# Optimization experiments

Hardware: AMD Instinct MI355X
Metric: run time of the kernel (lower is better)

Reference implementation:

```python
import jax, jax.numpy as jnp
import numpy as np

L, H, D, DH, DFF, V, P, T, R = 12, 12, 768, 64, 3072, 30522, 512, 2, 50
RAT_LAYER = 6  # original condition: 5 < idx < 7


def layer_norm(x, g, b, eps=1e-12):
    m = x.mean(-1, keepdims=True)
    v = ((x - m) ** 2).mean(-1, keepdims=True)
    return (x - m) / jnp.sqrt(v + eps) * g + b


def setup_inputs() -> dict:
    key = jax.random.key(0)
    ks = iter(jax.random.split(key, 20))
    def n(shape, s=0.02):
        return jax.random.normal(next(ks), shape, dtype=jnp.float32) * s
    inp = dict(
        input_ids=jax.random.randint(next(ks), (4, 512), 0, V, dtype=jnp.int32),
        relations=jax.random.randint(next(ks), (4, 512, 512), 0, R, dtype=jnp.int32),
        attention_mask=jnp.ones((4, 512), dtype=jnp.int32),
        word_emb=n((V, D)), pos_emb=n((P, D)), type_emb=n((T, D)),
        emb_ln_g=jnp.ones((D,)), emb_ln_b=jnp.zeros((D,)),
        Wq=n((L, D, D)), bq=jnp.zeros((L, D)), Wk=n((L, D, D)), bk=jnp.zeros((L, D)),
        Wv=n((L, D, D)), bv=jnp.zeros((L, D)), Wo=n((L, D, D)), bo=jnp.zeros((L, D)),
        ln1_g=jnp.ones((L, D)), ln1_b=jnp.zeros((L, D)),
        Wi=n((L, D, DFF)), bi=jnp.zeros((L, DFF)),
        Wf=n((L, DFF, D)), bf=jnp.zeros((L, D)),
        ln2_g=jnp.ones((L, D)), ln2_b=jnp.zeros((L, D)),
        key_rel=n((L, R, DH)), val_rel=n((L, R, DH)),
        pool_w=n((D, D)), pool_b=jnp.zeros((D,)),
    )
    return inp


def reference(input_ids, relations, attention_mask, word_emb, pos_emb, type_emb,
              emb_ln_g, emb_ln_b, Wq, bq, Wk, bk, Wv, bv, Wo, bo, ln1_g, ln1_b,
              Wi, bi, Wf, bf, ln2_g, ln2_b, key_rel, val_rel, pool_w, pool_b):
    B, S = input_ids.shape
    # BERT embeddings (token_type_ids = zeros as in module default)
    h = word_emb[input_ids] + pos_emb[jnp.arange(S)][None] + type_emb[0][None, None]
    h = layer_norm(h, emb_ln_g, emb_ln_b)
    ext_mask = (1.0 - attention_mask.astype(jnp.float32))[:, None, None, :] * -10000.0
    inv_sqrt_dh = np.float32(1.0 / np.sqrt(DH))
    for i in range(L):
        q = (h @ Wq[i] + bq[i]).reshape(B, S, H, DH).transpose(0, 2, 1, 3)
        k = (h @ Wk[i] + bk[i]).reshape(B, S, H, DH).transpose(0, 2, 1, 3)
        v = (h @ Wv[i] + bv[i]).reshape(B, S, H, DH).transpose(0, 2, 1, 3)
        scores = jnp.einsum('bhsd,bhtd->bhst', q, k)
        if i == RAT_LAYER:
            kr = key_rel[i][relations]            # [B,S,S,DH] gathered relation keys
            scores = scores + jnp.einsum('bhsd,bstd->bhst', q, kr)
        scores = scores * inv_sqrt_dh + ext_mask
        probs = jax.nn.softmax(scores, axis=-1)   # dropout = identity (eval)
        ctx = jnp.einsum('bhst,bhtd->bhsd', probs, v)
        if i == RAT_LAYER:
            vr = val_rel[i][relations]            # [B,S,S,DH] gathered relation values
            ctx = ctx + jnp.einsum('bhst,bstd->bhsd', probs, vr)
        ctx = ctx.transpose(0, 2, 1, 3).reshape(B, S, D)
        attn_out = layer_norm(ctx @ Wo[i] + bo[i] + h, ln1_g[i], ln1_b[i])
        ff = jax.nn.gelu(attn_out @ Wi[i] + bi[i], approximate=False)
        h = layer_norm(ff @ Wf[i] + bf[i] + attn_out, ln2_g[i], ln2_b[i])
    pooled = jnp.tanh(h[:, 0] @ pool_w + pool_b)
    return h, pooled
```

## Files before the change

kernel.cpp:

```cpp
#include <hip/hip_runtime.h>
#include <math.h>

typedef unsigned short u16;
typedef unsigned int   u32;
typedef __bf16  bf16x8 __attribute__((ext_vector_type(8)));
typedef float   f32x4  __attribute__((ext_vector_type(4)));
typedef u16     u16x8  __attribute__((ext_vector_type(8)));
typedef u16     u16x4  __attribute__((ext_vector_type(4)));

__device__ __forceinline__ u16 f2bf(float f) {
  u32 u = __builtin_bit_cast(u32, f);
  u32 r = (u + 0x7fffu + ((u >> 16) & 1u)) >> 16;
  return (u16)r;
}
__device__ __forceinline__ float bf2f(u16 h) {
  u32 u = ((u32)h) << 16;
  return __builtin_bit_cast(float, u);
}
__device__ __forceinline__ void gload16(const void* g, void* l) {
  __builtin_amdgcn_global_load_lds((const __attribute__((address_space(1))) void*)g,
                                   (__attribute__((address_space(3))) void*)l, 16, 0, 0);
}
__device__ __forceinline__ bf16x8 ld_bf8(const u16* p) {
  u16x8 v = *(const u16x8*)p;
  return __builtin_bit_cast(bf16x8, v);
}
__device__ __forceinline__ f32x4 mfma16(bf16x8 a, bf16x8 b, f32x4 c) {
  return __builtin_amdgcn_mfma_f32_16x16x32_bf16(a, b, c, 0, 0, 0);
}

struct ConvP {
  const float *wq, *wk, *wv, *wo, *wi, *wf;
  u16 *oqkv, *oo, *oi, *of;
  long doqkv, doo, doi, dof;
};
__global__ __launch_bounds__(256) void conv_weights(ConvP p, int l0) {
  int l = l0 + blockIdx.x / 6912;
  int t = blockIdx.x % 6912;
  const float* in; u16* out; int K, N, tn, tk;
  if (t < 1728) { int wh = t / 576, tt = t % 576;
    in = (wh==0 ? p.wq : (wh==1 ? p.wk : p.wv)) + (size_t)l*768*768;
    out = p.oqkv + (size_t)l*p.doqkv + (size_t)wh * 768 * 768;
    K = 768; N = 768; tn = tt % 24; tk = tt / 24;
  } else if (t < 2304) { int tt = t - 1728;
    in = p.wo + (size_t)l*768*768; out = p.oo + (size_t)l*p.doo;
    K=768;  N=768;  tn=tt%24; tk=tt/24;
  } else if (t < 4608) { int tt = t - 2304;
    in = p.wi + (size_t)l*768*3072; out = p.oi + (size_t)l*p.doi;
    K=768;  N=3072; tn=tt%96; tk=tt/96;
  } else { int tt = t - 4608;
    in = p.wf + (size_t)l*768*3072; out = p.of + (size_t)l*p.dof;
    K=3072; N=768;  tn=tt%24; tk=tt/24;
  }
  int n0 = tn*32, k0 = tk*32;
  __shared__ float tile[32][33];
  int tx = threadIdx.x, ty = threadIdx.y;
  float4 rv = *(const float4*)(in + (size_t)(k0 + ty) * N + n0 + tx*4);
  tile[ty][tx*4+0] = rv.x; tile[ty][tx*4+1] = rv.y;
  tile[ty][tx*4+2] = rv.z; tile[ty][tx*4+3] = rv.w;
  __syncthreads();
  u16x4 ov;
  ov[0] = f2bf(tile[tx*4+0][ty]); ov[1] = f2bf(tile[tx*4+1][ty]);
  ov[2] = f2bf(tile[tx*4+2][ty]); ov[3] = f2bf(tile[tx*4+3][ty]);
  *(u16x4*)(out + (size_t)(n0 + ty) * K + k0 + tx*4) = ov;
}

struct GP {
  const u16* A; const u16* B;
  int K, N;
  long sA, sB, sOut;
  const float* bias; const float* res;
  float* outF; u16* outB;
  const float* bq; const float* bk; const float* bv;
  u16* qO; u16* kO; u16* vO;
};

template<int BM, int BN, int WAVES, int EPI, int KS>
__global__ __launch_bounds__(WAVES*64) void gemm_bt(GP p) {
  constexpr int THREADS = WAVES * 64;
  constexpr int WC = WAVES / 2;
  constexpr int WM = BM / 2, WN = BN / WC, MR = WM / 16, NR = WN / 16;
  constexpr int AIT = BM * 64 / (THREADS * 8);
  constexpr int BIT = BN * 64 / (THREADS * 8);
  const int tid = threadIdx.x;
  const int wave = tid >> 6, lane = tid & 63;
  const int wr = wave / WC, wc = wave % WC;
  const int wm0 = wr * WM, wn0 = wc * WN;
  const int bn = blockIdx.x, bm = blockIdx.y, bz = blockIdx.z;
  const int K = p.K;
  const int kLen = K / KS;
  const int kBeg = (KS > 1) ? bz * kLen : 0;
  const u16* A  = p.A + ((KS > 1) ? 0 : (size_t)bz * p.sA);
  const u16* Bp = p.B + ((KS > 1) ? 0 : (size_t)bz * p.sB);
  const int rowA0 = bm * BM, colB0 = bn * BN;

  __shared__ __align__(16) u16 lds[(BM + BN) * 64];
  u16* Al = lds; u16* Bl = lds + BM * 64;

  f32x4 acc[MR][NR];
  #pragma unroll
  for (int i = 0; i < MR; ++i)
    #pragma unroll
    for (int j = 0; j < NR; ++j) acc[i][j] = f32x4{0.f,0.f,0.f,0.f};

  for (int kt = kBeg; kt < kBeg + kLen; kt += 64) {
    #pragma unroll
    for (int it = 0; it < AIT; ++it) {
      int e = tid * 8 + it * THREADS * 8;
      gload16(A + (size_t)(rowA0 + (e >> 6)) * K + kt + (e & 63), Al + e);
    }
    #pragma unroll
    for (int it = 0; it < BIT; ++it) {
      int e = tid * 8 + it * THREADS * 8;
      gload16(Bp + (size_t)(colB0 + (e >> 6)) * K + kt + (e & 63), Bl + e);
    }
    __syncthreads();
    #pragma unroll
    for (int ks = 0; ks < 2; ++ks) {
      bf16x8 av[MR]; bf16x8 bw[NR];
      #pragma unroll
      for (int mf = 0; mf < MR; ++mf)
        av[mf] = ld_bf8(Al + (wm0 + mf*16 + (lane&15))*64 + ks*32 + (lane>>4)*8);
      #pragma unroll
      for (int nf = 0; nf < NR; ++nf)
        bw[nf] = ld_bf8(Bl + (wn0 + nf*16 + (lane&15))*64 + ks*32 + (lane>>4)*8);
      #pragma unroll
      for (int mf = 0; mf < MR; ++mf)
        #pragma unroll
        for (int nf = 0; nf < NR; ++nf)
          acc[mf][nf] = mfma16(av[mf], bw[nf], acc[mf][nf]);
    }
    __syncthreads();
  }

  #pragma unroll
  for (int mf = 0; mf < MR; ++mf) {
    #pragma unroll
    for (int nf = 0; nf < NR; ++nf) {
      int col = colB0 + wn0 + nf*16 + (lane & 15);
      #pragma unroll
      for (int reg = 0; reg < 4; ++reg) {
        int row = rowA0 + wm0 + mf*16 + (lane >> 4)*4 + reg;
        float v = acc[mf][nf][reg];
        if constexpr (EPI == 0) {
          int wh = col / 768, cc = col % 768;
          int hh = cc >> 6, d = col & 63;
          int b = row >> 9, s = row & 511;
          const float* bias = wh==0 ? p.bq : (wh==1 ? p.bk : p.bv);
          u16 o = f2bf(v + bias[cc]);
          if (wh == 0)      p.qO[((((size_t)b*12 + hh)*512 + s) << 6) + d] = o;
          else if (wh == 1) p.kO[((((size_t)b*12 + hh)*512 + s) << 6) + d] = o;
          else              p.vO[((((size_t)b*12 + hh)*64  + d) << 9) + s] = o;
        } else if constexpr (EPI == 2) {
          p.outF[(size_t)bz * p.sOut + (size_t)row * p.N + col] = v;
        } else {
          float xg = v + p.bias[col];
          float gg = 0.5f * xg * (1.f + erff(xg * 0.70710678118f));
          p.outB[(size_t)row * p.N + col] = f2bf(gg);
        }
      }
    }
  }
}

template<int RAT>
__global__ __launch_bounds__(256) void flash_attn(
    const u16* __restrict__ q, const u16* __restrict__ k, const u16* __restrict__ v,
    const int* __restrict__ mask, u16* __restrict__ ctx,
    const float* __restrict__ qr, const int* __restrict__ rel,
    float* __restrict__ wbins) {
  const int head = blockIdx.x;
  const int bm = blockIdx.y;
  const int b = head / 12, hh = head % 12;
  const int tid = threadIdx.x, wave = tid >> 6, lane = tid & 63;
  const int wr = wave >> 1, wc = wave & 1;
  const int row0 = bm * 32;
  const u16* qb = q + (size_t)head * 512 * 64;
  const u16* kb = k + (size_t)head * 512 * 64;
  const u16* vb = v + (size_t)head * 64 * 512;

  __shared__ __align__(16) u16 Kl[2][64*64];
  __shared__ __align__(16) u16 Vl[2][64*64];
  __shared__ __align__(16) u16 pw[4][16*72];
  __shared__ float em_lds[512];
  __shared__ float mlb[2][16][2];
  __shared__ float qlds[RAT ? 32 : 1][RAT ? 52 : 1];
  __shared__ float wlds[RAT ? 2 : 1][RAT ? 32 : 1][RAT ? 50 : 1];
  __shared__ float scl[RAT ? 2 : 1][RAT ? 32 : 1];
  __shared__ float aex[RAT ? 32 : 1][RAT ? 3 : 1];

  for (int i = tid; i < 512; i += 256)
    em_lds[i] = -10000.f * (1.f - (float)mask[b*512 + i]);
  if constexpr (RAT) {
    for (int i = tid; i < 2*32*50; i += 256) ((float*)wlds)[i] = 0.f;
    for (int i = tid; i < 32*50; i += 256) {
      int rr = i % 50, sr = i / 50;
      qlds[sr][rr] = qr[((size_t)head*512 + row0 + sr)*50 + rr];
    }
  }

  const int qrow = row0 + wr*16 + (lane & 15);
  bf16x8 qf[2];
  qf[0] = ld_bf8(qb + (size_t)qrow*64 +      (lane>>4)*8);
  qf[1] = ld_bf8(qb + (size_t)qrow*64 + 32 + (lane>>4)*8);
  __syncthreads();

  f32x4 ctxacc[4];
  #pragma unroll
  for (int nf = 0; nf < 4; ++nf) ctxacc[nf] = f32x4{0.f,0.f,0.f,0.f};
  float mrun[4], lrun[4];
  #pragma unroll
  for (int r = 0; r < 4; ++r) { mrun[r] = -3.0e38f; lrun[r] = 0.f; }

  const int g = lane >> 4;
  for (int it = 0; it < 4; ++it) {
    #pragma unroll
    for (int j = 0; j < 2; ++j) {
      int s = j*256 + tid;
      int prow = s >> 3, c16 = (s & 7) ^ (prow & 7);
      int t0a = it*64, t0b = 256 + it*64;
      gload16(kb + (size_t)(t0a + prow)*64 + c16*8, Kl[0] + s*8);
      gload16(kb + (size_t)(t0b + prow)*64 + c16*8, Kl[1] + s*8);
      gload16(vb + (size_t)prow*512 + t0a + c16*8, Vl[0] + s*8);
      gload16(vb + (size_t)prow*512 + t0b + c16*8, Vl[1] + s*8);
    }
    __syncthreads();
    const int tbase = wc*256 + it*64;

    f32x4 s[4];
    #pragma unroll
    for (int nf = 0; nf < 4; ++nf) s[nf] = f32x4{0.f,0.f,0.f,0.f};
    #pragma unroll
    for (int ks = 0; ks < 2; ++ks)
      #pragma unroll
      for (int nf = 0; nf < 4; ++nf) {
        int row = nf*16 + (lane & 15);
        int c16 = (ks*4 + g) ^ (row & 7);
        bf16x8 kf = ld_bf8(Kl[wc] + row*64 + c16*8);
        s[nf] = mfma16(qf[ks], kf, s[nf]);
      }

    u32 rr4[RAT ? 4 : 1];
    if constexpr (RAT) {
      #pragma unroll
      for (int nf = 0; nf < 4; ++nf) {
        int tt = tbase + nf*16 + (lane & 15);
        u32 pack = 0;
        #pragma unroll
        for (int reg = 0; reg < 4; ++reg) {
          int rl = wr*16 + (lane>>4)*4 + reg;
          int rr = rel[((size_t)(b*512 + row0 + rl))*512 + tt];
          pack |= (u32)rr << (8*reg);
          s[nf][reg] += qlds[rl][rr];
        }
        rr4[nf] = pack;
      }
    }

    float em4[4];
    #pragma unroll
    for (int nf = 0; nf < 4; ++nf) em4[nf] = em_lds[tbase + nf*16 + (lane & 15)];

    float scale_[4];
    #pragma unroll
    for (int reg = 0; reg < 4; ++reg) {
      float pm = -3.0e38f;
      #pragma unroll
      for (int nf = 0; nf < 4; ++nf) {
        s[nf][reg] = s[nf][reg]*0.125f + em4[nf];
        pm = fmaxf(pm, s[nf][reg]);
      }
      #pragma unroll
      for (int o = 1; o < 16; o <<= 1) pm = fmaxf(pm, __shfl_xor(pm, o));
      float mnew = fmaxf(mrun[reg], pm);
      float sc = __expf(mrun[reg] - mnew);
      mrun[reg] = mnew;
      scale_[reg] = sc;
      float lsum = 0.f;
      #pragma unroll
      for (int nf = 0; nf < 4; ++nf) {
        float e = __expf(s[nf][reg] - mnew);
        s[nf][reg] = e;
        lsum += e;
      }
      #pragma unroll
      for (int o = 1; o < 16; o <<= 1) lsum += __shfl_xor(lsum, o);
      lrun[reg] = lrun[reg]*sc + lsum;
      if constexpr (RAT) {
        if ((lane & 15) == 0) scl[wc][wr*16 + (lane>>4)*4 + reg] = sc;
      }
    }

    if constexpr (RAT) {
      for (int i = lane; i < 16*50; i += 64) {
        int r = i / 50;
        wlds[wc][wr*16 + r][i % 50] *= scl[wc][wr*16 + r];
      }
      #pragma unroll
      for (int nf = 0; nf < 4; ++nf)
        #pragma unroll
        for (int reg = 0; reg < 4; ++reg) {
          int rl = wr*16 + (lane>>4)*4 + reg;
          int rr = (rr4[nf] >> (8*reg)) & 255;
          atomicAdd(&wlds[wc][rl][rr], s[nf][reg]);
        }
    }

    #pragma unroll
    for (int nf = 0; nf < 4; ++nf)
      #pragma unroll
      for (int reg = 0; reg < 4; ++reg) {
        int qq = (lane>>4)*4 + reg;
        pw[wave][qq*72 + nf*16 + (lane & 15)] = f2bf(s[nf][reg]);
      }

    #pragma unroll
    for (int nf = 0; nf < 4; ++nf)
      #pragma unroll
      for (int reg = 0; reg < 4; ++reg)
        ctxacc[nf][reg] *= scale_[reg];
    #pragma unroll
    for (int ks = 0; ks < 2; ++ks) {
      bf16x8 pf = ld_bf8(pw[wave] + (lane & 15)*72 + ks*32 + g*8);
      #pragma unroll
      for (int nf = 0; nf < 4; ++nf) {
        int row = nf*16 + (lane & 15);
        int c16 = (ks*4 + g) ^ (row & 7);
        bf16x8 vf = ld_bf8(Vl[wc] + row*64 + c16*8);
        ctxacc[nf] = mfma16(pf, vf, ctxacc[nf]);
      }
    }
    __syncthreads();
  }

  float* mergeF = (float*)pw;
  if (wc == 1) {
    #pragma unroll
    for (int nf = 0; nf < 4; ++nf)
      #pragma unroll
      for (int reg = 0; reg < 4; ++reg)
        mergeF[(wr*16 + (lane>>4)*4 + reg)*66 + nf*16 + (lane & 15)] = ctxacc[nf][reg];
    if ((lane & 15) == 0) {
      #pragma unroll
      for (int reg = 0; reg < 4; ++reg) {
        mlb[wr][(lane>>4)*4 + reg][0] = mrun[reg];
        mlb[wr][(lane>>4)*4 + reg][1] = lrun[reg];
      }
    }
  }
  __syncthreads();
  if (wc == 0) {
    float a1[4], a2[4], linv[4];
    #pragma unroll
    for (int reg = 0; reg < 4; ++reg) {
      int r = (lane>>4)*4 + reg;
      float m2 = mlb[wr][r][0], l2 = mlb[wr][r][1];
      float mn = fmaxf(mrun[reg], m2);
      a1[reg] = __expf(mrun[reg] - mn);
      a2[reg] = __expf(m2 - mn);
      linv[reg] = 1.f / (lrun[reg]*a1[reg] + l2*a2[reg]);
      if constexpr (RAT) {
        if ((lane & 15) == 0) {
          aex[wr*16 + r][0] = a1[reg];
          aex[wr*16 + r][1] = a2[reg];
          aex[wr*16 + r][2] = linv[reg];
        }
      }
    }
    #pragma unroll
    for (int nf = 0; nf < 4; ++nf)
      #pragma unroll
      for (int reg = 0; reg < 4; ++reg) {
        int r = wr*16 + (lane>>4)*4 + reg;
        int qg = row0 + r;
        int d = nf*16 + (lane & 15);
        float v2 = mergeF[r*66 + d];
        ctx[((size_t)(b*512 + qg))*768 + hh*64 + d] =
            f2bf((ctxacc[nf][reg]*a1[reg] + v2*a2[reg]) * linv[reg]);
      }
  }
  if constexpr (RAT) {
    __syncthreads();
    for (int i = tid; i < 32*50; i += 256) {
      int sr = i / 50, rr = i % 50;
      wbins[((size_t)head*512 + row0 + sr)*50 + rr] =
          (wlds[0][sr][rr]*aex[sr][0] + wlds[1][sr][rr]*aex[sr][1]) * aex[sr][2];
    }
  }
}

__global__ __launch_bounds__(256) void rat_qr(const u16* __restrict__ q,
    const float* __restrict__ kr, float* __restrict__ qr) {
  int idx = blockIdx.x * 256 + threadIdx.x;
  if (idx >= 24576 * 50) return;
  int r = idx % 50; size_t bhs = (size_t)idx / 50;
  const u16* qp = q + bhs * 64;
  const float* kp = kr + r * 64;
  float acc = 0.f;
  #pragma unroll
  for (int d = 0; d < 64; ++d) acc += bf2f(qp[d]) * kp[d];
  qr[idx] = acc;
}

__global__ __launch_bounds__(256) void rat_apply(const float* __restrict__ wbins,
    const float* __restrict__ vr, u16* __restrict__ ctx) {
  __shared__ float vrl[50*64];
  __shared__ float wl[32*50];
  int tid = threadIdx.x;
  int rows0 = blockIdx.x * 32;
  for (int i = tid; i < 50*64; i += 256) vrl[i] = vr[i];
  for (int i = tid; i < 32*50; i += 256) wl[i] = wbins[(size_t)rows0*50 + i];
  __syncthreads();
  int wave = tid >> 6, lane = tid & 63;
  #pragma unroll
  for (int i = 0; i < 8; ++i) {
    int r = wave*8 + i;
    size_t idx = (size_t)rows0 + r;
    float acc = 0.f;
    #pragma unroll
    for (int j = 0; j < 50; ++j) acc += wl[r*50 + j] * vrl[j*64 + lane];
    int s = (int)(idx & 511); size_t bh = idx >> 9;
    int b = (int)(bh / 12), hh = (int)(bh % 12);
    u16* cp = ctx + ((size_t)(b*512 + s))*768 + hh*64 + lane;
    *cp = f2bf(bf2f(*cp) + acc);
  }
}

__global__ __launch_bounds__(256) void embed_ln(const int* __restrict__ ids,
    const float* __restrict__ we, const float* __restrict__ pe, const float* __restrict__ te,
    const float* __restrict__ g, const float* __restrict__ b,
    float* __restrict__ hF, u16* __restrict__ hB) {
  int row = blockIdx.x, tid = threadIdx.x;
  int s = row & 511;
  int id = ids[row];
  float x[3];
  #pragma unroll
  for (int j = 0; j < 3; ++j) {
    int d = tid + j*256;
    x[j] = we[(size_t)id*768 + d] + pe[(size_t)s*768 + d] + te[d];
  }
  __shared__ float red[4];
  float sm = x[0] + x[1] + x[2];
  #pragma unroll
  for (int o = 32; o; o >>= 1) sm += __shfl_xor(sm, o);
  if (!(tid & 63)) red[tid >> 6] = sm;
  __syncthreads();
  float mean = (red[0]+red[1]+red[2]+red[3]) * (1.f/768.f);
  __syncthreads();
  float q = 0.f;
  #pragma unroll
  for (int j = 0; j < 3; ++j) { float d = x[j] - mean; q += d*d; }
  #pragma unroll
  for (int o = 32; o; o >>= 1) q += __shfl_xor(q, o);
  if (!(tid & 63)) red[tid >> 6] = q;
  __syncthreads();
  float inv = rsqrtf((red[0]+red[1]+red[2]+red[3]) * (1.f/768.f) + 1e-12f);
  #pragma unroll
  for (int j = 0; j < 3; ++j) {
    int d = tid + j*256;
    float y = (x[j] - mean) * inv * g[d] + b[d];
    hF[(size_t)row*768 + d] = y;
    hB[(size_t)row*768 + d] = f2bf(y);
  }
}

__global__ __launch_bounds__(256) void ln_fused(const float* __restrict__ p0,
    const float* __restrict__ p1, const float* __restrict__ p2, const float* __restrict__ p3,
    int np, const float* __restrict__ bias, const float* __restrict__ res,
    const float* __restrict__ g, const float* __restrict__ b,
    float* __restrict__ oF, u16* __restrict__ oB) {
  int row = blockIdx.x, tid = threadIdx.x;
  size_t base = (size_t)row * 768;
  float v[3];
  #pragma unroll
  for (int j = 0; j < 3; ++j) {
    int d = tid + j*256;
    float x = p0[base + d];
    if (np > 1) x += p1[base + d];
    if (np > 2) x += p2[base + d];
    if (np > 3) x += p3[base + d];
    v[j] = x + bias[d] + res[base + d];
  }
  __shared__ float red[4];
  float sm = v[0] + v[1] + v[2];
  #pragma unroll
  for (int o = 32; o; o >>= 1) sm += __shfl_xor(sm, o);
  if (!(tid & 63)) red[tid >> 6] = sm;
  __syncthreads();
  float mean = (red[0]+red[1]+red[2]+red[3]) * (1.f/768.f);
  __syncthreads();
  float q = 0.f;
  #pragma unroll
  for (int j = 0; j < 3; ++j) { float d = v[j] - mean; q += d*d; }
  #pragma unroll
  for (int o = 32; o; o >>= 1) q += __shfl_xor(q, o);
  if (!(tid & 63)) red[tid >> 6] = q;
  __syncthreads();
  float inv = rsqrtf((red[0]+red[1]+red[2]+red[3]) * (1.f/768.f) + 1e-12f);
  #pragma unroll
  for (int j = 0; j < 3; ++j) {
    int d = tid + j*256;
    float y = (v[j] - mean) * inv * g[d] + b[d];
    oF[base + d] = y;
    oB[base + d] = f2bf(y);
  }
}

__global__ __launch_bounds__(256) void pooler_k(const float* __restrict__ h,
    const float* __restrict__ w, const float* __restrict__ bias, float* __restrict__ out) {
  int b = blockIdx.x, tid = threadIdx.x;
  __shared__ float hr[768];
  for (int i = tid; i < 768; i += 256) hr[i] = h[((size_t)b*512)*768 + i];
  __syncthreads();
  float a0 = 0.f, a1 = 0.f, a2 = 0.f;
  for (int kk = 0; kk < 768; ++kk) {
    float hv = hr[kk];
    const float* wr = w + (size_t)kk*768;
    a0 += hv * wr[tid]; a1 += hv * wr[tid+256]; a2 += hv * wr[tid+512];
  }
  out[(size_t)b*768 + tid]       = tanhf(a0 + bias[tid]);
  out[(size_t)b*768 + tid + 256] = tanhf(a1 + bias[tid+256]);
  out[(size_t)b*768 + tid + 512] = tanhf(a2 + bias[tid+512]);
}

__global__ __launch_bounds__(256) void copy_out(const float* __restrict__ in, float* __restrict__ out) {
  size_t i = ((size_t)blockIdx.x * 256 + threadIdx.x) * 4;
  *(float4*)(out + i) = *(const float4*)(in + i);
}

extern "C" void kernel_launch(void* const* d_in, const int* in_sizes, int n_in,
                              void* d_out, int out_size, void* d_ws, size_t ws_size,
                              hipStream_t stream) {
  const int*   ids   = (const int*)d_in[0];
  const int*   rel   = (const int*)d_in[1];
  const int*   amask = (const int*)d_in[2];
  const float* we    = (const float*)d_in[3];
  const float* pe    = (const float*)d_in[4];
  const float* te    = (const float*)d_in[5];
  const float* eg    = (const float*)d_in[6];
  const float* ebb   = (const float*)d_in[7];
  const float* Wq    = (const float*)d_in[8];
  const float* bq    = (const float*)d_in[9];
  const float* Wk    = (const float*)d_in[10];
  const float* bk    = (const float*)d_in[11];
  const float* Wv    = (const float*)d_in[12];
  const float* bv    = (const float*)d_in[13];
  const float* Wo    = (const float*)d_in[14];
  const float* bo    = (const float*)d_in[15];
  const float* g1    = (const float*)d_in[16];
  const float* b1    = (const float*)d_in[17];
  const float* Wi    = (const float*)d_in[18];
  const float* bi    = (const float*)d_in[19];
  const float* Wf    = (const float*)d_in[20];
  const float* bfp   = (const float*)d_in[21];
  const float* g2    = (const float*)d_in[22];
  const float* b2    = (const float*)d_in[23];
  const float* krel  = (const float*)d_in[24];
  const float* vrel  = (const float*)d_in[25];
  const float* pwp   = (const float*)d_in[26];
  const float* pbp   = (const float*)d_in[27];
  (void)in_sizes; (void)n_in; (void)out_size;

  char* ws = (char*)d_ws;
  size_t off = 0;
  auto take = [&](size_t bytes) { char* p = ws + off; off += (bytes + 255) & ~(size_t)255; return p; };
  float* hF   = (float*)take((size_t)2048*768*4);
  u16*   hB   = (u16*)take((size_t)2048*768*2);
  float* atF  = (float*)take((size_t)2048*768*4);
  u16*   atB  = (u16*)take((size_t)2048*768*2);
  u16*   qB   = (u16*)take((size_t)2048*768*2);
  u16*   kB   = (u16*)take((size_t)2048*768*2);
  u16*   vB   = (u16*)take((size_t)2048*768*2);
  u16*   ctxB = (u16*)take((size_t)2048*768*2);
  float* tmpF = (float*)take((size_t)4*2048*768*4);
  u16*   ffB  = (u16*)take((size_t)2048*3072*2);
  float* qrF  = (float*)take((size_t)24576*50*4);
  float* wbF  = (float*)take((size_t)24576*50*4);
  const size_t PSTRIDE = (size_t)2048*768;

  const size_t WQKV = (size_t)2304*768, WWO = (size_t)768*768;
  const size_t WWI = (size_t)768*3072, WWF = (size_t)3072*768;
  const size_t wLayerBytes = (WQKV + WWO + WWI + WWF) * 2;
  const bool preall = (off + 12*wLayerBytes + 65536 <= ws_size);
  const int NL = preall ? 12 : 1;
  u16* wqkvB = (u16*)take(WQKV*2*NL);
  u16* woB   = (u16*)take(WWO*2*NL);
  u16* wiB   = (u16*)take(WWI*2*NL);
  u16* wfB   = (u16*)take(WWF*2*NL);

  ConvP cp{Wq, Wk, Wv, Wo, Wi, Wf, wqkvB, woB, wiB, wfB,
           preall ? (long)WQKV : 0, preall ? (long)WWO : 0,
           preall ? (long)WWI : 0, preall ? (long)WWF : 0};

  embed_ln<<<2048, 256, 0, stream>>>(ids, we, pe, te, eg, ebb, hF, hB);
  if (preall) conv_weights<<<12*6912, dim3(8,32), 0, stream>>>(cp, 0);

  for (int l = 0; l < 12; ++l) {
    if (!preall) conv_weights<<<6912, dim3(8,32), 0, stream>>>(cp, l);
    const u16* wqkv_l = wqkvB + (size_t)l*cp.doqkv;
    const u16* wo_l   = woB   + (size_t)l*cp.doo;
    const u16* wi_l   = wiB   + (size_t)l*cp.doi;
    const u16* wf_l   = wfB   + (size_t)l*cp.dof;

    GP pq{}; pq.A = hB; pq.B = wqkv_l; pq.K = 768; pq.N = 2304;
    pq.bq = bq + l*768; pq.bk = bk + l*768; pq.bv = bv + l*768;
    pq.qO = qB; pq.kO = kB; pq.vO = vB;
    gemm_bt<64,128,4,0,1><<<dim3(18,32,1), 256, 0, stream>>>(pq);

    if (l == 6) {
      rat_qr<<<4800, 256, 0, stream>>>(qB, krel + 6*50*64, qrF);
      flash_attn<1><<<dim3(48,16), 256, 0, stream>>>(qB, kB, vB, amask, ctxB, qrF, rel, wbF);
      rat_apply<<<768, 256, 0, stream>>>(wbF, vrel + 6*50*64, ctxB);
    } else {
      flash_attn<0><<<dim3(48,16), 256, 0, stream>>>(qB, kB, vB, amask, ctxB, nullptr, nullptr, nullptr);
    }

    GP po{}; po.A = ctxB; po.B = wo_l; po.K = 768; po.N = 768; po.sOut = PSTRIDE;
    po.outF = tmpF;
    gemm_bt<64,128,4,2,2><<<dim3(6,32,2), 256, 0, stream>>>(po);
    ln_fused<<<2048, 256, 0, stream>>>(tmpF, tmpF + PSTRIDE, nullptr, nullptr, 2,
                                       bo + l*768, hF, g1 + l*768, b1 + l*768, atF, atB);

    GP pf1{}; pf1.A = atB; pf1.B = wi_l; pf1.K = 768; pf1.N = 3072;
    pf1.bias = bi + (size_t)l*3072; pf1.outB = ffB;
    gemm_bt<64,128,4,3,1><<<dim3(24,32,1), 256, 0, stream>>>(pf1);

    GP pf2{}; pf2.A = ffB; pf2.B = wf_l; pf2.K = 3072; pf2.N = 768; pf2.sOut = PSTRIDE;
    pf2.outF = tmpF;
    gemm_bt<64,128,4,2,4><<<dim3(6,32,4), 256, 0, stream>>>(pf2);
    ln_fused<<<2048, 256, 0, stream>>>(tmpF, tmpF + PSTRIDE, tmpF + 2*PSTRIDE, tmpF + 3*PSTRIDE, 4,
                                       bfp + l*768, atF, g2 + l*768, b2 + l*768, hF, hB);
  }

  copy_out<<<1536, 256, 0, stream>>>(hF, (float*)d_out);
  pooler_k<<<4, 256, 0, stream>>>(hF, pwp, pbp, (float*)d_out + (size_t)2048*768);
}
```

Baseline: 1.703 ms.

## Fuse relation-key projection into RAT flash attention and enlarge weight-convert tiles

Removes the separate rat_qr kernel: the relation keys are converted to bf16 in LDS (reusing the pw buffer) and q·key_rel is computed with MFMA inside the RAT flash-attention block, writing directly into qlds. This eliminates one launch and the global round trip of the q·kr scores, with slightly lower precision because key_rel is now bf16. Separately, the weight transpose/convert kernel now uses 64x64 tiles with 4 iterations per thread, launching a quarter as many blocks.

```diff
diff --git a/kernel.cpp b/kernel.cpp
--- a/kernel.cpp
+++ b/kernel.cpp
@@ -35,34 +35,43 @@
   long doqkv, doo, doi, dof;
 };
 __global__ __launch_bounds__(256) void conv_weights(ConvP p, int l0) {
-  int l = l0 + blockIdx.x / 6912;
-  int t = blockIdx.x % 6912;
+  int l = l0 + blockIdx.x / 1728;
+  int t = blockIdx.x % 1728;
   const float* in; u16* out; int K, N, tn, tk;
-  if (t < 1728) { int wh = t / 576, tt = t % 576;
+  if (t < 432) { int wh = t / 144, tt = t % 144;
     in = (wh==0 ? p.wq : (wh==1 ? p.wk : p.wv)) + (size_t)l*768*768;
     out = p.oqkv + (size_t)l*p.doqkv + (size_t)wh * 768 * 768;
-    K = 768; N = 768; tn = tt % 24; tk = tt / 24;
-  } else if (t < 2304) { int tt = t - 1728;
+    K = 768; N = 768; tn = tt % 12; tk = tt / 12;
+  } else if (t < 576) { int tt = t - 432;
     in = p.wo + (size_t)l*768*768; out = p.oo + (size_t)l*p.doo;
-    K=768;  N=768;  tn=tt%24; tk=tt/24;
-  } else if (t < 4608) { int tt = t - 2304;
+    K=768;  N=768;  tn=tt%12; tk=tt/12;
+  } else if (t < 1152) { int tt = t - 576;
     in = p.wi + (size_t)l*768*3072; out = p.oi + (size_t)l*p.doi;
-    K=768;  N=3072; tn=tt%96; tk=tt/96;
-  } else { int tt = t - 4608;
+    K=768;  N=3072; tn=tt%48; tk=tt/48;
+  } else { int tt = t - 1152;
     in = p.wf + (size_t)l*768*3072; out = p.of + (size_t)l*p.dof;
-    K=3072; N=768;  tn=tt%24; tk=tt/24;
-  }
-  int n0 = tn*32, k0 = tk*32;
-  __shared__ float tile[32][33];
-  int tx = threadIdx.x, ty = threadIdx.y;
-  float4 rv = *(const float4*)(in + (size_t)(k0 + ty) * N + n0 + tx*4);
-  tile[ty][tx*4+0] = rv.x; tile[ty][tx*4+1] = rv.y;
-  tile[ty][tx*4+2] = rv.z; tile[ty][tx*4+3] = rv.w;
-  __syncthreads();
-  u16x4 ov;
-  ov[0] = f2bf(tile[tx*4+0][ty]); ov[1] = f2bf(tile[tx*4+1][ty]);
-  ov[2] = f2bf(tile[tx*4+2][ty]); ov[3] = f2bf(tile[tx*4+3][ty]);
-  *(u16x4*)(out + (size_t)(n0 + ty) * K + k0 + tx*4) = ov;
+    K=3072; N=768;  tn=tt%12; tk=tt/12;
+  }
+  int n0 = tn*64, k0 = tk*64;
+  __shared__ float tile[64][65];
+  int tid = threadIdx.x;
+  int tx = tid & 15, ry = tid >> 4;
+  #pragma unroll
+  for (int j = 0; j < 4; ++j) {
+    int kk = j*16 + ry;
+    float4 rv = *(const float4*)(in + (size_t)(k0 + kk) * N + n0 + tx*4);
+    tile[kk][tx*4+0] = rv.x; tile[kk][tx*4+1] = rv.y;
+    tile[kk][tx*4+2] = rv.z; tile[kk][tx*4+3] = rv.w;
+  }
+  __syncthreads();
+  #pragma unroll
+  for (int j = 0; j < 4; ++j) {
+    int nn = j*16 + ry;
+    u16x4 ov;
+    ov[0] = f2bf(tile[tx*4+0][nn]); ov[1] = f2bf(tile[tx*4+1][nn]);
+    ov[2] = f2bf(tile[tx*4+2][nn]); ov[3] = f2bf(tile[tx*4+3][nn]);
+    *(u16x4*)(out + (size_t)(n0 + nn) * K + k0 + tx*4) = ov;
+  }
 }
 
 struct GP {
@@ -167,7 +176,7 @@
 __global__ __launch_bounds__(256) void flash_attn(
     const u16* __restrict__ q, const u16* __restrict__ k, const u16* __restrict__ v,
     const int* __restrict__ mask, u16* __restrict__ ctx,
-    const float* __restrict__ qr, const int* __restrict__ rel,
+    const float* __restrict__ kr, const int* __restrict__ rel,
     float* __restrict__ wbins) {
   const int head = blockIdx.x;
   const int bm = blockIdx.y;
@@ -191,19 +200,40 @@
 
   for (int i = tid; i < 512; i += 256)
     em_lds[i] = -10000.f * (1.f - (float)mask[b*512 + i]);
+  u16* Krl = (u16*)pw;
   if constexpr (RAT) {
     for (int i = tid; i < 2*32*50; i += 256) ((float*)wlds)[i] = 0.f;
-    for (int i = tid; i < 32*50; i += 256) {
-      int rr = i % 50, sr = i / 50;
-      qlds[sr][rr] = qr[((size_t)head*512 + row0 + sr)*50 + rr];
+    for (int i = tid; i < 64*64; i += 256) {
+      int r = i >> 6, c = i & 63;
+      Krl[i] = (r < 50) ? f2bf(kr[r*64 + c]) : (u16)0;
     }
   }
 
   const int qrow = row0 + wr*16 + (lane & 15);
+  const int g = lane >> 4;
   bf16x8 qf[2];
-  qf[0] = ld_bf8(qb + (size_t)qrow*64 +      (lane>>4)*8);
-  qf[1] = ld_bf8(qb + (size_t)qrow*64 + 32 + (lane>>4)*8);
-  __syncthreads();
+  qf[0] = ld_bf8(qb + (size_t)qrow*64 +      g*8);
+  qf[1] = ld_bf8(qb + (size_t)qrow*64 + 32 + g*8);
+  __syncthreads();
+
+  if constexpr (RAT) {
+    #pragma unroll
+    for (int nf = 0; nf < 2; ++nf) {
+      f32x4 a = f32x4{0.f,0.f,0.f,0.f};
+      #pragma unroll
+      for (int ks = 0; ks < 2; ++ks) {
+        bf16x8 krf = ld_bf8(Krl + (wc*32 + nf*16 + (lane&15))*64 + ks*32 + g*8);
+        a = mfma16(qf[ks], krf, a);
+      }
+      int rr = wc*32 + nf*16 + (lane & 15);
+      if (rr < 50) {
+        #pragma unroll
+        for (int reg = 0; reg < 4; ++reg)
+          qlds[wr*16 + g*4 + reg][rr] = a[reg];
+      }
+    }
+    __syncthreads();
+  }
 
   f32x4 ctxacc[4];
   #pragma unroll
@@ -212,7 +242,6 @@
   #pragma unroll
   for (int r = 0; r < 4; ++r) { mrun[r] = -3.0e38f; lrun[r] = 0.f; }
 
-  const int g = lane >> 4;
   for (int it = 0; it < 4; ++it) {
     #pragma unroll
     for (int j = 0; j < 2; ++j) {
@@ -248,7 +277,7 @@
         u32 pack = 0;
         #pragma unroll
         for (int reg = 0; reg < 4; ++reg) {
-          int rl = wr*16 + (lane>>4)*4 + reg;
+          int rl = wr*16 + g*4 + reg;
           int rr = rel[((size_t)(b*512 + row0 + rl))*512 + tt];
           pack |= (u32)rr << (8*reg);
           s[nf][reg] += qlds[rl][rr];
@@ -287,7 +316,7 @@
       for (int o = 1; o < 16; o <<= 1) lsum += __shfl_xor(lsum, o);
       lrun[reg] = lrun[reg]*sc + lsum;
       if constexpr (RAT) {
-        if ((lane & 15) == 0) scl[wc][wr*16 + (lane>>4)*4 + reg] = sc;
+        if ((lane & 15) == 0) scl[wc][wr*16 + g*4 + reg] = sc;
       }
     }
 
@@ -300,7 +329,7 @@
       for (int nf = 0; nf < 4; ++nf)
         #pragma unroll
         for (int reg = 0; reg < 4; ++reg) {
-          int rl = wr*16 + (lane>>4)*4 + reg;
+          int rl = wr*16 + g*4 + reg;
           int rr = (rr4[nf] >> (8*reg)) & 255;
           atomicAdd(&wlds[wc][rl][rr], s[nf][reg]);
         }
@@ -310,7 +339,7 @@
     for (int nf = 0; nf < 4; ++nf)
       #pragma unroll
       for (int reg = 0; reg < 4; ++reg) {
-        int qq = (lane>>4)*4 + reg;
+        int qq = g*4 + reg;
         pw[wave][qq*72 + nf*16 + (lane & 15)] = f2bf(s[nf][reg]);
       }
 
@@ -339,12 +368,12 @@
     for (int nf = 0; nf < 4; ++nf)
       #pragma unroll
       for (int reg = 0; reg < 4; ++reg)
-        mergeF[(wr*16 + (lane>>4)*4 + reg)*66 + nf*16 + (lane & 15)] = ctxacc[nf][reg];
+        mergeF[(wr*16 + g*4 + reg)*66 + nf*16 + (lane & 15)] = ctxacc[nf][reg];
     if ((lane & 15) == 0) {
       #pragma unroll
       for (int reg = 0; reg < 4; ++reg) {
-        mlb[wr][(lane>>4)*4 + reg][0] = mrun[reg];
-        mlb[wr][(lane>>4)*4 + reg][1] = lrun[reg];
+        mlb[wr][g*4 + reg][0] = mrun[reg];
+        mlb[wr][g*4 + reg][1] = lrun[reg];
       }
     }
   }
@@ -353,7 +382,7 @@
     float a1[4], a2[4], linv[4];
     #pragma unroll
     for (int reg = 0; reg < 4; ++reg) {
-      int r = (lane>>4)*4 + reg;
+      int r = g*4 + reg;
       float m2 = mlb[wr][r][0], l2 = mlb[wr][r][1];
       float mn = fmaxf(mrun[reg], m2);
       a1[reg] = __expf(mrun[reg] - mn);
@@ -371,7 +400,7 @@
     for (int nf = 0; nf < 4; ++nf)
       #pragma unroll
       for (int reg = 0; reg < 4; ++reg) {
-        int r = wr*16 + (lane>>4)*4 + reg;
+        int r = wr*16 + g*4 + reg;
         int qg = row0 + r;
         int d = nf*16 + (lane & 15);
         float v2 = mergeF[r*66 + d];
@@ -387,19 +416,6 @@
           (wlds[0][sr][rr]*aex[sr][0] + wlds[1][sr][rr]*aex[sr][1]) * aex[sr][2];
     }
   }
-}
-
-__global__ __launch_bounds__(256) void rat_qr(const u16* __restrict__ q,
-    const float* __restrict__ kr, float* __restrict__ qr) {
-  int idx = blockIdx.x * 256 + threadIdx.x;
-  if (idx >= 24576 * 50) return;
-  int r = idx % 50; size_t bhs = (size_t)idx / 50;
-  const u16* qp = q + bhs * 64;
-  const float* kp = kr + r * 64;
-  float acc = 0.f;
-  #pragma unroll
-  for (int d = 0; d < 64; ++d) acc += bf2f(qp[d]) * kp[d];
-  qr[idx] = acc;
 }
 
 __global__ __launch_bounds__(256) void rat_apply(const float* __restrict__ wbins,
@@ -574,7 +590,6 @@
   u16*   ctxB = (u16*)take((size_t)2048*768*2);
   float* tmpF = (float*)take((size_t)4*2048*768*4);
   u16*   ffB  = (u16*)take((size_t)2048*3072*2);
-  float* qrF  = (float*)take((size_t)24576*50*4);
   float* wbF  = (float*)take((size_t)24576*50*4);
   const size_t PSTRIDE = (size_t)2048*768;
 
@@ -593,10 +608,10 @@
            preall ? (long)WWI : 0, preall ? (long)WWF : 0};
 
   embed_ln<<<2048, 256, 0, stream>>>(ids, we, pe, te, eg, ebb, hF, hB);
-  if (preall) conv_weights<<<12*6912, dim3(8,32), 0, stream>>>(cp, 0);
+  if (preall) conv_weights<<<12*1728, 256, 0, stream>>>(cp, 0);
 
   for (int l = 0; l < 12; ++l) {
-    if (!preall) conv_weights<<<6912, dim3(8,32), 0, stream>>>(cp, l);
+    if (!preall) conv_weights<<<1728, 256, 0, stream>>>(cp, l);
     const u16* wqkv_l = wqkvB + (size_t)l*cp.doqkv;
     const u16* wo_l   = woB   + (size_t)l*cp.doo;
     const u16* wi_l   = wiB   + (size_t)l*cp.doi;
@@ -608,11 +623,12 @@
     gemm_bt<64,128,4,0,1><<<dim3(18,32,1), 256, 0, stream>>>(pq);
 
     if (l == 6) {
-      rat_qr<<<4800, 256, 0, stream>>>(qB, krel + 6*50*64, qrF);
-      flash_attn<1><<<dim3(48,16), 256, 0, stream>>>(qB, kB, vB, amask, ctxB, qrF, rel, wbF);
+      flash_attn<1><<<dim3(48,16), 256, 0, stream>>>(qB, kB, vB, amask, ctxB,
+                                                     krel + 6*50*64, rel, wbF);
       rat_apply<<<768, 256, 0, stream>>>(wbF, vrel + 6*50*64, ctxB);
     } else {
-      flash_attn<0><<<dim3(48,16), 256, 0, stream>>>(qB, kB, vB, amask, ctxB, nullptr, nullptr, nullptr);
+      flash_attn<0><<<dim3(48,16), 256, 0, stream>>>(qB, kB, vB, amask, ctxB,
+                                                     nullptr, nullptr, nullptr);
     }
 
     GP po{}; po.A = ctxB; po.B = wo_l; po.K = 768; po.N = 768; po.sOut = PSTRIDE;
```

Measured after the change: 1.666 ms. 1.02x faster.
